# Kernel optimization log

Hardware: AMD Instinct MI355X
Metric: run time of the kernel (lower is better)

The kernel has to match this reference:

```python
import jax, jax.numpy as jnp
import numpy as np

B, DM, H, W = 2, 96, 48, 48
E = 192          # d_expand == d_inner
R, N = 6, 16     # delta_rank, d_state


def conv2d(x, w, b, groups=1, pad=0):
    out = jax.lax.conv_general_dilated(
        x, w, window_strides=(1, 1), padding=[(pad, pad), (pad, pad)],
        dimension_numbers=("NCHW", "OIHW", "NCHW"), feature_group_count=groups)
    return out + b[None, :, None, None]


def setup_inputs() -> dict:
    key = jax.random.key(0)
    ks = jax.random.split(key, 24)
    f = lambda k, shape, s: jax.random.normal(k, shape, jnp.float32) * s
    inp = {
        "x": jax.random.normal(ks[0], (B, DM, H, W), jnp.float32),
        "in_proj_w": f(ks[1], (2 * E, DM), 0.05),
        "conv_w": f(ks[2], (E, 1, 3, 3), 0.2),
        "conv_b": f(ks[3], (E,), 0.1),
        "x_proj_w": f(ks[4], (4, R + 2 * N, E), 0.01),
        "dt_proj_w": f(ks[5], (4, E, R), 0.01),
        "dt_proj_b": jnp.full((4, E), -9.0) + f(ks[6], (4, E), 0.1),
        "A_log": jnp.tile(jnp.log(jnp.arange(1, N + 1, dtype=jnp.float32))[None, None, :], (4, E, 1)),
        "Ds": jnp.ones((4, E), jnp.float32),
        "ln_g": jnp.ones(E, jnp.float32), "ln_b": jnp.zeros(E, jnp.float32),
        "c1_w": f(ks[7], (2 * E, E, 1, 1), 0.05), "c1_b": jnp.zeros(2 * E),
        "bn1_g": jnp.ones(2 * E), "bn1_b": jnp.zeros(2 * E), "bn1_m": jnp.zeros(2 * E), "bn1_v": jnp.ones(2 * E),
        "c2_w": f(ks[8], (2 * E, 1, 3, 3), 0.2), "c2_b": jnp.zeros(2 * E),
        "bn2_g": jnp.ones(2 * E), "bn2_b": jnp.zeros(2 * E), "bn2_m": jnp.zeros(2 * E), "bn2_v": jnp.ones(2 * E),
        "c3_w": f(ks[9], (E // 2, 2 * E, 1, 1), 0.05), "c3_b": jnp.zeros(E // 2),
        "se1_w": f(ks[10], (E // 4, E // 2), 0.1), "se1_b": jnp.zeros(E // 4),
        "se2_w": f(ks[11], (E // 2, E // 4), 0.1), "se2_b": jnp.zeros(E // 2),
    }
    return inp


def reference(x, in_proj_w, conv_w, conv_b, x_proj_w, dt_proj_w, dt_proj_b,
              A_log, Ds, ln_g, ln_b,
              c1_w, c1_b, bn1_g, bn1_b, bn1_m, bn1_v,
              c2_w, c2_b, bn2_g, bn2_b, bn2_m, bn2_v,
              c3_w, c3_b, se1_w, se1_b, se2_w, se2_b):
    Bs, _, Hs, Ws = x.shape
    L = Hs * Ws
    # in projection (Linear over channel dim), split x/z gates
    xz = jnp.einsum("bchw,oc->bohw", x, in_proj_w)
    xi, z = jnp.split(xz, 2, axis=1)
    # depthwise conv + SiLU
    xi = jax.nn.silu(conv2d(xi, conv_w, conv_b, groups=E, pad=1))
    # ---- selective scan (4-direction cross scan, cumsum formulation) ----
    xf = xi.reshape(Bs, E, L)
    xt = jnp.swapaxes(xi, 2, 3).reshape(Bs, E, L)
    xs = jnp.stack([xf, xf[..., ::-1], xt, xt[..., ::-1]], axis=1)  # [B,4,E,L]
    dbc = jnp.einsum("bkcl,krc->bkrl", xs, x_proj_w)                # [B,4,R+2N,L]
    dlt, b, c = dbc[:, :, :R], dbc[:, :, R:R + N], dbc[:, :, R + N:]
    dlt = jnp.einsum("bkrl,kdr->bkdl", dlt, dt_proj_w) + dt_proj_b[None, :, :, None]
    dlt = jax.nn.softplus(dlt)                                      # [B,4,E,L]
    dA = dlt[..., None] * A_log[None, :, :, None, :]                # [B,4,E,L,N]
    phi = jnp.exp(-jnp.cumsum(dA, axis=3))
    dbx = dlt[..., None] * jnp.swapaxes(b, 2, 3)[:, :, None] * xs[..., None]  # [B,4,E,L,N]
    h = phi * jnp.cumsum(dbx / (phi + 1e-12), axis=3)
    y = jnp.einsum("bkdln,bknl->bkdl", h, c) + Ds[None, :, :, None]  # [B,4,E,L]
    # ---- cross merge ----
    y1 = y[:, 0]
    y2 = y[:, 1, :, ::-1]
    y3 = jnp.swapaxes(y[:, 2].reshape(Bs, E, Ws, Hs), 2, 3).reshape(Bs, E, L)
    y4 = jnp.swapaxes(y[:, 3, :, ::-1].reshape(Bs, E, Ws, Hs), 2, 3).reshape(Bs, E, L)
    ys = (y1 + y2 + y3 + y4).reshape(Bs, E, Hs, Ws)
    # layernorm over channels
    yn = jnp.moveaxis(ys, 1, -1)
    mu = yn.mean(-1, keepdims=True)
    var = yn.var(-1, keepdims=True)
    yn = (yn - mu) / jnp.sqrt(var + 1e-5) * ln_g + ln_b
    u = jnp.moveaxis(yn, -1, 1) * z
    # ---- EFFN ----
    def bn(t, g, bb, m, v):
        return (t - m[None, :, None, None]) / jnp.sqrt(v + 1e-5)[None, :, None, None] * g[None, :, None, None] + bb[None, :, None, None]
    t = jax.nn.relu(bn(conv2d(u, c1_w, c1_b), bn1_g, bn1_b, bn1_m, bn1_v))
    t = jax.nn.relu(bn(conv2d(t, c2_w, c2_b, groups=2 * E, pad=1), bn2_g, bn2_b, bn2_m, bn2_v))
    t = conv2d(t, c3_w, c3_b)
    # squeeze-excitation: t + t * sigmoid(fc(relu(fc(avgpool(t)))))
    s = t.mean((2, 3))
    s = jax.nn.relu(s @ se1_w.T + se1_b)
    s = jax.nn.sigmoid(s @ se2_w.T + se2_b)
    return t + t * s[:, :, None, None]
```

## Files before the change

### kernel.cpp

```cpp
#include <hip/hip_runtime.h>
#include <hip/hip_bf16.h>

#define LTOT 2304
#define ECH  192
#define NCH  16
#define CCH  192
#define SCH  12

__device__ __forceinline__ int permS(int k, int l) {
  if (k == 0) return l;
  if (k == 1) return LTOT - 1 - l;
  int m = (k == 2) ? l : (LTOT - 1 - l);
  return (m % 48) * 48 + (m / 48);
}

__device__ __forceinline__ float sp_fast(float x) {
  float t = __expf(x);
  return (t <= 0.018f) ? t * fmaf(t, fmaf(t, 0.33333334f, -0.5f), 1.f) : log1pf(t);
}

__global__ __launch_bounds__(256) void k1_inproj(const float* __restrict__ x,
                                                 const float* __restrict__ W,
                                                 float* __restrict__ xi_pre,
                                                 float* __restrict__ z) {
  const int l0 = blockIdx.x * 32;
  const int o0 = blockIdx.y * 64;
  const int b  = blockIdx.z;
  __shared__ __align__(16) float xs[96 * 34];
  __shared__ __align__(16) float Wl[96 * 68];
  const int tid = threadIdx.x;
  for (int idx = tid; idx < 96 * 32; idx += 256) {
    int i = idx & 31, cc = idx >> 5;
    xs[cc * 34 + i] = x[(b * 96 + cc) * LTOT + l0 + i];
  }
  for (int idx = tid; idx < 64 * 96; idx += 256) {
    int r = idx / 96, cc = idx - r * 96;
    Wl[cc * 68 + r] = W[(o0 + r) * 96 + cc];
  }
  __syncthreads();
  const int lane = tid & 63, w = tid >> 6;
  const int jj = lane & 15, rqq = lane >> 4;
  const int rbase = 16 * w + 4 * rqq;
  float acc[2][4];
#pragma unroll
  for (int p = 0; p < 2; ++p)
#pragma unroll
    for (int t = 0; t < 4; ++t) acc[p][t] = 0.f;
#pragma unroll 4
  for (int cc = 0; cc < 96; ++cc) {
    const float4 wv = *(const float4*)&Wl[cc * 68 + rbase];
    const float2 xv = *(const float2*)&xs[cc * 34 + 2 * jj];
    acc[0][0] = fmaf(wv.x, xv.x, acc[0][0]); acc[0][1] = fmaf(wv.y, xv.x, acc[0][1]);
    acc[0][2] = fmaf(wv.z, xv.x, acc[0][2]); acc[0][3] = fmaf(wv.w, xv.x, acc[0][3]);
    acc[1][0] = fmaf(wv.x, xv.y, acc[1][0]); acc[1][1] = fmaf(wv.y, xv.y, acc[1][1]);
    acc[1][2] = fmaf(wv.z, xv.y, acc[1][2]); acc[1][3] = fmaf(wv.w, xv.y, acc[1][3]);
  }
  __syncthreads();
  float* ol = xs;
#pragma unroll
  for (int t = 0; t < 4; ++t) {
    ol[(rbase + t) * 33 + 2 * jj]     = acc[0][t];
    ol[(rbase + t) * 33 + 2 * jj + 1] = acc[1][t];
  }
  __syncthreads();
  for (int idx = tid; idx < 32 * 64; idx += 256) {
    int r = idx & 63, pos = idx >> 6;
    float v = ol[r * 33 + pos];
    int o = o0 + r, l = l0 + pos;
    if (o < ECH) xi_pre[(b * LTOT + l) * ECH + o] = v;
    else         z[(b * LTOT + l) * ECH + (o - ECH)] = v;
  }
}

__global__ __launch_bounds__(256) void k2_dwconv(const float* __restrict__ xi_pre,
                                                 const float* __restrict__ cw,
                                                 const float* __restrict__ cb,
                                                 float* __restrict__ xi) {
  int g = blockIdx.x * 256 + threadIdx.x;
  if (g >= 2 * LTOT * ECH) return;
  int e = g % ECH; int l = (g / ECH) % LTOT; int b = g / (ECH * LTOT);
  int h = l / 48, wq = l % 48;
  float acc = cb[e];
#pragma unroll
  for (int kh = 0; kh < 3; ++kh) {
    int hh = h + kh - 1; if (hh < 0 || hh >= 48) continue;
#pragma unroll
    for (int kw = 0; kw < 3; ++kw) {
      int ww = wq + kw - 1; if (ww < 0 || ww >= 48) continue;
      acc = fmaf(cw[e * 9 + kh * 3 + kw], xi_pre[(b * LTOT + hh * 48 + ww) * ECH + e], acc);
    }
  }
  xi[g] = acc / (1.f + __expf(-acc));
}

__global__ __launch_bounds__(256) void k3_xproj(const float* __restrict__ xi,
                                                const float* __restrict__ xw,
                                                float* __restrict__ dl6g,
                                                float* __restrict__ bT,
                                                float* __restrict__ cT) {
  const int l0 = blockIdx.x * 32;
  const int k  = blockIdx.y;
  const int b  = blockIdx.z;
  __shared__ __align__(16) float xs[96 * 34];
  __shared__ __align__(16) float Wl[192 * 40];
  const int tid = threadIdx.x;
  const float* wsrc = xw + k * 38 * ECH;
  for (int idx = tid; idx < 38 * 192; idx += 256) {
    int r = idx / 192, cc = idx - r * 192;
    Wl[cc * 40 + r] = wsrc[idx];
  }
  const int lane = tid & 63, w = tid >> 6;
  const int jj = lane & 15;
  const int rq = w * 4 + (lane >> 4);
  const int rqc = rq < 9 ? rq : 9;
  const int j0 = 2 * jj;
  float a00 = 0.f, a01 = 0.f, a02 = 0.f, a03 = 0.f;
  float a10 = 0.f, a11 = 0.f, a12 = 0.f, a13 = 0.f;
  for (int kc = 0; kc < 2; ++kc) {
    __syncthreads();
    for (int idx = tid; idx < 32 * 96; idx += 256) {
      int j = idx / 96, cc = idx - j * 96;
      int s = permS(k, l0 + j);
      xs[cc * 34 + j] = xi[(b * LTOT + s) * ECH + kc * 96 + cc];
    }
    __syncthreads();
#pragma unroll 4
    for (int cc = 0; cc < 96; ++cc) {
      const float2 xv = *(const float2*)&xs[cc * 34 + j0];
      const float4 wv = *(const float4*)&Wl[(kc * 96 + cc) * 40 + 4 * rqc];
      a00 = fmaf(wv.x, xv.x, a00); a01 = fmaf(wv.y, xv.x, a01);
      a02 = fmaf(wv.z, xv.x, a02); a03 = fmaf(wv.w, xv.x, a03);
      a10 = fmaf(wv.x, xv.y, a10); a11 = fmaf(wv.y, xv.y, a11);
      a12 = fmaf(wv.z, xv.y, a12); a13 = fmaf(wv.w, xv.y, a13);
    }
  }
  const int bk = b * 4 + k;
  if (rq < 10) {
    float av[2][4] = {{a00, a01, a02, a03}, {a10, a11, a12, a13}};
#pragma unroll
    for (int t = 0; t < 4; ++t) {
      int r = 4 * rq + t;
      if (r >= 38) continue;
#pragma unroll
      for (int p = 0; p < 2; ++p) {
        int j = j0 + p;
        float v = av[p][t];
        if (r < 6)       dl6g[((bk * LTOT) + l0 + j) * 6 + r] = v;
        else if (r < 22) bT[((bk * LTOT) + l0 + j) * NCH + (r - 6)] = v;
        else             cT[((bk * LTOT) + l0 + j) * NCH + (r - 22)] = v;
      }
    }
  }
}

__global__ __launch_bounds__(256) void k4a_scan1(const float* __restrict__ dl6g,
                                                 const float* __restrict__ xi,
                                                 const float* __restrict__ bT,
                                                 const float* __restrict__ Alog,
                                                 const float* __restrict__ dtw,
                                                 const float* __restrict__ dtb,
                                                 float* __restrict__ q,
                                                 float* __restrict__ Ts) {
  const int cb = blockIdx.x;
  const int db = blockIdx.y;
  const int bk = blockIdx.z;
  const int b = bk >> 2, k = bk & 3;
  const int l0 = cb * 48;
  __shared__ __align__(16) float2 sdx[48 * 64];
  __shared__ __align__(16) float  sb[48 * NCH];
  const int tid = threadIdx.x;
  const int dd = tid & 63, cg = tid >> 6;
  const int dg = db * 64 + dd;
  float b6 = dtb[k * ECH + dg];
  float w6[6];
  {
    const float2* d2 = (const float2*)(dtw + (k * ECH + dg) * 6);
    float2 u0 = d2[0], u1 = d2[1], u2 = d2[2];
    w6[0] = u0.x; w6[1] = u0.y; w6[2] = u1.x; w6[3] = u1.y; w6[4] = u2.x; w6[5] = u2.y;
  }
  for (int idx = tid; idx < 48 * NCH; idx += 256) sb[idx] = bT[(bk * LTOT + l0) * NCH + idx];
  for (int e = tid; e < 48 * 64; e += 256) {
    int s = e >> 6;
    const float* d6 = dl6g + (bk * LTOT + l0 + s) * 6;
    float xa = b6;
#pragma unroll
    for (int r = 0; r < 6; ++r) xa = fmaf(w6[r], d6[r], xa);
    float dl = sp_fast(xa);
    int sp = permS(k, l0 + s);
    sdx[s * 64 + dd] = make_float2(dl, xi[(b * LTOT + sp) * ECH + dg]);
  }
  float C1[16], h[16];
#pragma unroll
  for (int n = 0; n < 16; ++n) {
    C1[n] = Alog[(k * ECH + dg) * NCH + n];
    h[n] = 0.f;
  }
  __syncthreads();
  float Tsum = 0.f;
  for (int i = 0; i < SCH; ++i) {
    int j = cg * SCH + i;
    float2 dx = sdx[j * 64 + dd];
    float dl = dx.x;
    float u  = dl * dx.y;
    Tsum += dl;
    const float4* bb4 = (const float4*)(sb + j * NCH);
    float4 q0 = bb4[0], q1 = bb4[1], q2 = bb4[2], q3 = bb4[3];
    float bbl[16] = {q0.x, q0.y, q0.z, q0.w, q1.x, q1.y, q1.z, q1.w,
                     q2.x, q2.y, q2.z, q2.w, q3.x, q3.y, q3.z, q3.w};
    if (dl <= 0.018f) {
#pragma unroll
      for (int n = 0; n < 16; ++n) {
        float xn = C1[n] * dl;
        float e = fmaf(xn, fmaf(xn, fmaf(xn, -(1.f / 6.f), 0.5f), -1.f), 1.f);
        h[n] = fmaf(e, h[n], u * bbl[n]);
      }
    } else {
#pragma unroll
      for (int n = 0; n < 16; ++n) {
        float e = __expf(-C1[n] * dl);
        h[n] = fmaf(e, h[n], u * bbl[n]);
      }
    }
  }
  const int c = cb * 4 + cg;
  float4* qp = (float4*)(q + ((bk * CCH + c) * ECH + dg) * NCH);
  qp[0] = make_float4(h[0], h[1], h[2], h[3]);
  qp[1] = make_float4(h[4], h[5], h[6], h[7]);
  qp[2] = make_float4(h[8], h[9], h[10], h[11]);
  qp[3] = make_float4(h[12], h[13], h[14], h[15]);
  Ts[(bk * CCH + c) * ECH + dg] = Tsum;
}

__global__ __launch_bounds__(256) void k4b_comb(const float* __restrict__ Alog,
                                                const float* __restrict__ Ts,
                                                float* __restrict__ q) {
  int t = blockIdx.x * 256 + threadIdx.x;
  if (t >= 8 * ECH * NCH) return;
  int n = t & 15, d = (t >> 4) % ECH, bk = t / (NCH * ECH);
  int k = bk & 3;
  float A = Alog[(k * ECH + d) * NCH + n];
  float h = 0.f;
#pragma unroll 4
  for (int c = 0; c < CCH; ++c) {
    int base = ((bk * CCH + c) * ECH + d) * NCH + n;
    float qc = q[base];
    q[base] = h;
    float xv = A * Ts[(bk * CCH + c) * ECH + d];
    float P = (xv <= 0.05f)
                  ? fmaf(xv, fmaf(xv, fmaf(xv, -(1.f / 6.f), 0.5f), -1.f), 1.f)
                  : __expf(-xv);
    h = fmaf(P, h, qc);
  }
}

__global__ __launch_bounds__(256) void k4c_scan2(const float* __restrict__ dl6g,
                                                 const float* __restrict__ xi,
                                                 const float* __restrict__ bT,
                                                 const float* __restrict__ cT,
                                                 const float* __restrict__ Alog,
                                                 const float* __restrict__ dtw,
                                                 const float* __restrict__ dtb,
                                                 const float* __restrict__ hin,
                                                 float* __restrict__ yd) {
  const int cb = blockIdx.x;
  const int db = blockIdx.y;
  const int bk = blockIdx.z;
  const int b = bk >> 2, k = bk & 3;
  const int l0 = cb * 48;
  __shared__ __align__(16) float2 sdx[48 * 64];
  __shared__ __align__(16) float  sb[48 * NCH];
  __shared__ __align__(16) float  sc[48 * NCH];
  const int tid = threadIdx.x;
  const int dd = tid & 63, cg = tid >> 6;
  const int dg = db * 64 + dd;
  float b6 = dtb[k * ECH + dg];
  float w6[6];
  {
    const float2* d2 = (const float2*)(dtw + (k * ECH + dg) * 6);
    float2 u0 = d2[0], u1 = d2[1], u2 = d2[2];
    w6[0] = u0.x; w6[1] = u0.y; w6[2] = u1.x; w6[3] = u1.y; w6[4] = u2.x; w6[5] = u2.y;
  }
  for (int idx = tid; idx < 48 * NCH; idx += 256) {
    sb[idx] = bT[(bk * LTOT + l0) * NCH + idx];
    sc[idx] = cT[(bk * LTOT + l0) * NCH + idx];
  }
  for (int e = tid; e < 48 * 64; e += 256) {
    int s = e >> 6;
    const float* d6 = dl6g + (bk * LTOT + l0 + s) * 6;
    float xa = b6;
#pragma unroll
    for (int r = 0; r < 6; ++r) xa = fmaf(w6[r], d6[r], xa);
    float dl = sp_fast(xa);
    int sp = permS(k, l0 + s);
    sdx[s * 64 + dd] = make_float2(dl, xi[(b * LTOT + sp) * ECH + dg]);
  }
  float C1[16], h[16];
  const int c = cb * 4 + cg;
  const float4* hp = (const float4*)(hin + ((bk * CCH + c) * ECH + dg) * NCH);
  {
    float4 h0 = hp[0], h1 = hp[1], h2 = hp[2], h3 = hp[3];
    h[0]=h0.x; h[1]=h0.y; h[2]=h0.z; h[3]=h0.w;
    h[4]=h1.x; h[5]=h1.y; h[6]=h1.z; h[7]=h1.w;
    h[8]=h2.x; h[9]=h2.y; h[10]=h2.z; h[11]=h2.w;
    h[12]=h3.x; h[13]=h3.y; h[14]=h3.z; h[15]=h3.w;
  }
#pragma unroll
  for (int n = 0; n < 16; ++n) C1[n] = Alog[(k * ECH + dg) * NCH + n];
  float* ydk = yd + (b * 4 + k) * LTOT * ECH;
  __syncthreads();
  for (int i = 0; i < SCH; ++i) {
    int j = cg * SCH + i;
    float2 dx = sdx[j * 64 + dd];
    float dl = dx.x;
    float u  = dl * dx.y;
    const float4* bb4 = (const float4*)(sb + j * NCH);
    float4 q0 = bb4[0], q1 = bb4[1], q2 = bb4[2], q3 = bb4[3];
    float bbl[16] = {q0.x, q0.y, q0.z, q0.w, q1.x, q1.y, q1.z, q1.w,
                     q2.x, q2.y, q2.z, q2.w, q3.x, q3.y, q3.z, q3.w};
    if (dl <= 0.018f) {
#pragma unroll
      for (int n = 0; n < 16; ++n) {
        float xn = C1[n] * dl;
        float e = fmaf(xn, fmaf(xn, fmaf(xn, -(1.f / 6.f), 0.5f), -1.f), 1.f);
        h[n] = fmaf(e, h[n], u * bbl[n]);
      }
    } else {
#pragma unroll
      for (int n = 0; n < 16; ++n) {
        float e = __expf(-C1[n] * dl);
        h[n] = fmaf(e, h[n], u * bbl[n]);
      }
    }
    const float4* cc4 = (const float4*)(sc + j * NCH);
    float4 c0 = cc4[0], c1 = cc4[1], c2 = cc4[2], c3 = cc4[3];
    float ccl[16] = {c0.x, c0.y, c0.z, c0.w, c1.x, c1.y, c1.z, c1.w,
                     c2.x, c2.y, c2.z, c2.w, c3.x, c3.y, c3.z, c3.w};
    float y = 0.f;
#pragma unroll
    for (int n = 0; n < 16; ++n) y = fmaf(h[n], ccl[n], y);
    int sp = permS(k, l0 + j);
    ydk[sp * ECH + dg] = y;
  }
}

__global__ __launch_bounds__(256) void k5_ln(const float* __restrict__ yd,
                                             const float* __restrict__ Ds,
                                             const float* __restrict__ lng,
                                             const float* __restrict__ lnb,
                                             float* __restrict__ zu) {
  int p = blockIdx.x * 4 + (threadIdx.x >> 6);
  int lane = threadIdx.x & 63;
  int b = (p >= LTOT) ? 1 : 0;
  int l = p - b * LTOT;
  const float* y0 = yd + (b * 4) * LTOT * ECH + l * ECH;
  float vd[3], sd[3];
#pragma unroll
  for (int t = 0; t < 3; ++t) {
    int d = lane + t * 64;
    vd[t] = ((y0[d] + y0[LTOT * ECH + d]) + y0[2 * LTOT * ECH + d]) + y0[3 * LTOT * ECH + d];
    sd[t] = Ds[d] + Ds[ECH + d] + Ds[2 * ECH + d] + Ds[3 * ECH + d];
  }
  float s1 = vd[0] + vd[1] + vd[2];
  float s2 = sd[0] + sd[1] + sd[2];
#pragma unroll
  for (int off = 32; off > 0; off >>= 1) {
    s1 += __shfl_xor(s1, off, 64);
    s2 += __shfl_xor(s2, off, 64);
  }
  float mean_dot = s1 * (1.f / 192.f);
  float mean_sd  = s2 * (1.f / 192.f);
  float dev[3];
  float ss = 0.f;
#pragma unroll
  for (int t = 0; t < 3; ++t) {
    dev[t] = (vd[t] - mean_dot) + (sd[t] - mean_sd);
    ss = fmaf(dev[t], dev[t], ss);
  }
#pragma unroll
  for (int off = 32; off > 0; off >>= 1) ss += __shfl_xor(ss, off, 64);
  float rstd = 1.f / sqrtf(ss * (1.f / 192.f) + 1e-5f);
#pragma unroll
  for (int t = 0; t < 3; ++t) {
    int d = lane + t * 64;
    float yn = (dev[t] * rstd) * lng[d] + lnb[d];
    zu[p * ECH + d] = yn * zu[p * ECH + d];
  }
}

__global__ __launch_bounds__(256) void k6_c1(const float* __restrict__ u,
                                             const float* __restrict__ W,
                                             const float* __restrict__ c1b,
                                             const float* __restrict__ g1,
                                             const float* __restrict__ b1,
                                             const float* __restrict__ m1,
                                             const float* __restrict__ v1,
                                             float* __restrict__ t1,
                                             float* __restrict__ se) {
  const int l0 = blockIdx.x * 32;
  const int o0 = blockIdx.y * 64;
  const int b  = blockIdx.z;
  const int tid = threadIdx.x;
  if (blockIdx.x == 0 && blockIdx.y == 0 && blockIdx.z == 0 && tid < 192) se[tid] = 0.f;
  __shared__ __align__(16) float xs[96 * 34];
  __shared__ __align__(16) float Wl[96 * 68];
  const int lane = tid & 63, w = tid >> 6;
  const int jj = lane & 15, rqq = lane >> 4;
  const int rbase = 16 * w + 4 * rqq;
  float acc[2][4];
#pragma unroll
  for (int p = 0; p < 2; ++p)
#pragma unroll
    for (int t = 0; t < 4; ++t) acc[p][t] = 0.f;
  for (int kc = 0; kc < 2; ++kc) {
    if (kc) __syncthreads();
    for (int idx = tid; idx < 32 * 96; idx += 256) {
      int cc = idx % 96, i = idx / 96;
      xs[cc * 34 + i] = u[(b * LTOT + l0 + i) * ECH + kc * 96 + cc];
    }
    for (int idx = tid; idx < 64 * 96; idx += 256) {
      int r = idx / 96, cc = idx - r * 96;
      Wl[cc * 68 + r] = W[(o0 + r) * ECH + kc * 96 + cc];
    }
    __syncthreads();
#pragma unroll 4
    for (int cc = 0; cc < 96; ++cc) {
      const float4 wv = *(const float4*)&Wl[cc * 68 + rbase];
      const float2 xv = *(const float2*)&xs[cc * 34 + 2 * jj];
      acc[0][0] = fmaf(wv.x, xv.x, acc[0][0]); acc[0][1] = fmaf(wv.y, xv.x, acc[0][1]);
      acc[0][2] = fmaf(wv.z, xv.x, acc[0][2]); acc[0][3] = fmaf(wv.w, xv.x, acc[0][3]);
      acc[1][0] = fmaf(wv.x, xv.y, acc[1][0]); acc[1][1] = fmaf(wv.y, xv.y, acc[1][1]);
      acc[1][2] = fmaf(wv.z, xv.y, acc[1][2]); acc[1][3] = fmaf(wv.w, xv.y, acc[1][3]);
    }
  }
#pragma unroll
  for (int t = 0; t < 4; ++t) {
    int o = o0 + rbase + t;
    float sc = g1[o] / sqrtf(v1[o] + 1e-5f);
    float bias = (c1b[o] - m1[o]) * sc + b1[o];
#pragma unroll
    for (int p = 0; p < 2; ++p) acc[p][t] = fmaxf(fmaf(acc[p][t], sc, bias), 0.f);
  }
  __syncthreads();
  float* ol = xs;
#pragma unroll
  for (int t = 0; t < 4; ++t) {
    ol[(rbase + t) * 33 + 2 * jj]     = acc[0][t];
    ol[(rbase + t) * 33 + 2 * jj + 1] = acc[1][t];
  }
  __syncthreads();
  for (int idx = tid; idx < 32 * 64; idx += 256) {
    int pos = idx & 31, r = idx >> 5;
    t1[(b * 384 + o0 + r) * LTOT + l0 + pos] = ol[r * 33 + pos];
  }
}

__global__ __launch_bounds__(256) void k7_dw2(const float* __restrict__ t1,
                                              const float* __restrict__ cw,
                                              const float* __restrict__ cb,
                                              const float* __restrict__ g2,
                                              const float* __restrict__ b2,
                                              const float* __restrict__ m2,
                                              const float* __restrict__ v2,
                                              float* __restrict__ t2) {
  int g = blockIdx.x * 256 + threadIdx.x;
  if (g >= 2 * LTOT * 384) return;
  int l = g % LTOT; int o = (g / LTOT) % 384; int b = g / (LTOT * 384);
  int h = l / 48, wq = l % 48;
  const float* src = t1 + (b * 384 + o) * LTOT;
  float acc = cb[o];
#pragma unroll
  for (int kh = 0; kh < 3; ++kh) {
    int hh = h + kh - 1; if (hh < 0 || hh >= 48) continue;
#pragma unroll
    for (int kw = 0; kw < 3; ++kw) {
      int ww = wq + kw - 1; if (ww < 0 || ww >= 48) continue;
      acc = fmaf(cw[o * 9 + kh * 3 + kw], src[hh * 48 + ww], acc);
    }
  }
  float sc = g2[o] / sqrtf(v2[o] + 1e-5f);
  float val = (acc - m2[o]) * sc + b2[o];
  t2[g] = fmaxf(val, 0.f);
}

__global__ __launch_bounds__(256) void k8_c3(const float* __restrict__ t2,
                                             const float* __restrict__ W,
                                             const float* __restrict__ c3b,
                                             float* __restrict__ t3,
                                             float* __restrict__ se) {
  const int l0 = blockIdx.x * 32;
  const int r0 = blockIdx.y * 32;
  const int b  = blockIdx.z;
  __shared__ __align__(16) float Wl[384 * 34];
  __shared__ __align__(16) float xs[192 * 34];
  const int tid = threadIdx.x;
  const int lane = tid & 63, w = tid >> 6;
  const int jj = lane & 15, rqq = lane >> 4;
  const int rloc = 8 * w + 2 * rqq;
  for (int idx = tid; idx < 32 * 384; idx += 256) {
    int r = idx / 384, cc = idx - r * 384;
    Wl[cc * 34 + r] = W[(r0 + r) * 384 + cc];
  }
  float acc[2][2];
  acc[0][0] = acc[0][1] = acc[1][0] = acc[1][1] = 0.f;
  for (int kc = 0; kc < 2; ++kc) {
    if (kc) __syncthreads();
    for (int idx = tid; idx < 192 * 32; idx += 256) {
      int i = idx & 31, cc = idx >> 5;
      xs[cc * 34 + i] = t2[(b * 384 + kc * 192 + cc) * LTOT + l0 + i];
    }
    __syncthreads();
#pragma unroll 4
    for (int cc = 0; cc < 192; ++cc) {
      const float2 wv = *(const float2*)&Wl[(kc * 192 + cc) * 34 + rloc];
      const float2 xv = *(const float2*)&xs[cc * 34 + 2 * jj];
      acc[0][0] = fmaf(wv.x, xv.x, acc[0][0]); acc[0][1] = fmaf(wv.y, xv.x, acc[0][1]);
      acc[1][0] = fmaf(wv.x, xv.y, acc[1][0]); acc[1][1] = fmaf(wv.y, xv.y, acc[1][1]);
    }
  }
  {
    float b0 = c3b[r0 + rloc], b1v = c3b[r0 + rloc + 1];
    acc[0][0] += b0; acc[1][0] += b0; acc[0][1] += b1v; acc[1][1] += b1v;
  }
#pragma unroll
  for (int t = 0; t < 2; ++t) {
    float v = acc[0][t] + acc[1][t];
    v += __shfl_xor(v, 1); v += __shfl_xor(v, 2);
    v += __shfl_xor(v, 4); v += __shfl_xor(v, 8);
    if (jj == 0) atomicAdd(&se[b * 96 + r0 + rloc + t], v);
  }
  __syncthreads();
  float* ol = xs;
#pragma unroll
  for (int t = 0; t < 2; ++t) {
    ol[(rloc + t) * 33 + 2 * jj]     = acc[0][t];
    ol[(rloc + t) * 33 + 2 * jj + 1] = acc[1][t];
  }
  __syncthreads();
  for (int idx = tid; idx < 32 * 32; idx += 256) {
    int pos = idx & 31, r = idx >> 5;
    t3[(b * 96 + r0 + r) * LTOT + l0 + pos] = ol[r * 33 + pos];
  }
}

__global__ __launch_bounds__(256) void k9_out(const float* __restrict__ t3,
                                              const float* __restrict__ se,
                                              const float* __restrict__ w1,
                                              const float* __restrict__ sb1,
                                              const float* __restrict__ w2,
                                              const float* __restrict__ sb2,
                                              float* __restrict__ out) {
  __shared__ float sm[192];
  __shared__ float s1[96];
  __shared__ float smul[192];
  int t = threadIdx.x;
  if (t < 192) sm[t] = se[t] * (1.f / 2304.f);
  __syncthreads();
  if (t < 96) {
    int b = t / 48, i = t % 48;
    float a = sb1[i];
#pragma unroll 4
    for (int m = 0; m < 96; ++m) a = fmaf(w1[i * 96 + m], sm[b * 96 + m], a);
    s1[t] = fmaxf(a, 0.f);
  }
  __syncthreads();
  if (t < 192) {
    int b = t / 96, j = t % 96;
    float a = sb2[j];
#pragma unroll 4
    for (int i = 0; i < 48; ++i) a = fmaf(w2[j * 48 + i], s1[b * 48 + i], a);
    smul[t] = 1.f + 1.f / (1.f + __expf(-a));
  }
  __syncthreads();
  int g = blockIdx.x * 256 + t;
  if (g < 2 * 96 * LTOT) out[g] = t3[g] * smul[g / LTOT];
}

extern "C" void kernel_launch(void* const* d_in, const int* in_sizes, int n_in,
                              void* d_out, int out_size, void* d_ws, size_t ws_size,
                              hipStream_t stream) {
  const float* x     = (const float*)d_in[0];
  const float* inw   = (const float*)d_in[1];
  const float* convw = (const float*)d_in[2];
  const float* convb = (const float*)d_in[3];
  const float* xpw   = (const float*)d_in[4];
  const float* dtw   = (const float*)d_in[5];
  const float* dtb   = (const float*)d_in[6];
  const float* Alog  = (const float*)d_in[7];
  const float* Ds    = (const float*)d_in[8];
  const float* lng   = (const float*)d_in[9];
  const float* lnb   = (const float*)d_in[10];
  const float* c1w   = (const float*)d_in[11];
  const float* c1b   = (const float*)d_in[12];
  const float* bn1g  = (const float*)d_in[13];
  const float* bn1b  = (const float*)d_in[14];
  const float* bn1m  = (const float*)d_in[15];
  const float* bn1v  = (const float*)d_in[16];
  const float* c2w   = (const float*)d_in[17];
  const float* c2b   = (const float*)d_in[18];
  const float* bn2g  = (const float*)d_in[19];
  const float* bn2b  = (const float*)d_in[20];
  const float* bn2m  = (const float*)d_in[21];
  const float* bn2v  = (const float*)d_in[22];
  const float* c3w   = (const float*)d_in[23];
  const float* c3b   = (const float*)d_in[24];
  const float* se1w  = (const float*)d_in[25];
  const float* se1b  = (const float*)d_in[26];
  const float* se2w  = (const float*)d_in[27];
  const float* se2b  = (const float*)d_in[28];

  float* ws = (float*)d_ws;
  float* xi_pre = ws;
  float* z      = ws + 884736;
  float* xi     = ws + 1769472;
  float* dl6g   = ws + 2654208;
  float* bT     = ws + 2764800;
  float* cT     = ws + 3354624;
  float* q      = ws + 3944448;
  float* Ts     = ws + 13381632;
  float* se     = ws + 13676544;
  float* yd     = ws + 13676736;
  float* t1 = yd;
  float* t2 = yd + 1769472;
  float* t3 = q;

  k1_inproj<<<dim3(72, 6, 2), 256, 0, stream>>>(x, inw, xi_pre, z);
  k2_dwconv<<<3456, 256, 0, stream>>>(xi_pre, convw, convb, xi);
  k3_xproj<<<dim3(72, 4, 2), 256, 0, stream>>>(xi, xpw, dl6g, bT, cT);
  k4a_scan1<<<dim3(48, 3, 8), 256, 0, stream>>>(dl6g, xi, bT, Alog, dtw, dtb, q, Ts);
  k4b_comb<<<96, 256, 0, stream>>>(Alog, Ts, q);
  k4c_scan2<<<dim3(48, 3, 8), 256, 0, stream>>>(dl6g, xi, bT, cT, Alog, dtw, dtb, q, yd);
  k5_ln<<<1152, 256, 0, stream>>>(yd, Ds, lng, lnb, z);
  k6_c1<<<dim3(72, 6, 2), 256, 0, stream>>>(z, c1w, c1b, bn1g, bn1b, bn1m, bn1v, t1, se);
  k7_dw2<<<6912, 256, 0, stream>>>(t1, c2w, c2b, bn2g, bn2b, bn2m, bn2v, t2);
  k8_c3<<<dim3(72, 3, 2), 256, 0, stream>>>(t2, c3w, c3b, t3, se);
  k9_out<<<1728, 256, 0, stream>>>(t3, se, se1w, se1b, se2w, se2b, (float*)d_out);
}
```

Measured before the change: 341.6 us.

## Parallelize chunk-combine scan across chunk segments with two-level prefix in shared memory

The chunk-state combine kernel previously ran one thread per (bk,d,n) and walked all 192 chunks serially, using only 96 blocks. It now launches one block per (d,bk), splits the 192 chunks into 16 segments of 12 per thread, computes local decay products and partial states, combines segment prefixes through shared memory, then rewrites the carried-in states. This is meant to remove the long serial dependency chain and the low occupancy of that kernel. The cost is extra recomputation per thread, a serial loop over earlier segments, and strided global accesses that coalesce less well across d.

```diff
diff --git a/kernel.cpp b/kernel.cpp
--- a/kernel.cpp
+++ b/kernel.cpp
@@ -234,22 +234,42 @@
 __global__ __launch_bounds__(256) void k4b_comb(const float* __restrict__ Alog,
                                                 const float* __restrict__ Ts,
                                                 float* __restrict__ q) {
-  int t = blockIdx.x * 256 + threadIdx.x;
-  if (t >= 8 * ECH * NCH) return;
-  int n = t & 15, d = (t >> 4) % ECH, bk = t / (NCH * ECH);
-  int k = bk & 3;
-  float A = Alog[(k * ECH + d) * NCH + n];
-  float h = 0.f;
-#pragma unroll 4
-  for (int c = 0; c < CCH; ++c) {
-    int base = ((bk * CCH + c) * ECH + d) * NCH + n;
-    float qc = q[base];
-    q[base] = h;
-    float xv = A * Ts[(bk * CCH + c) * ECH + d];
-    float P = (xv <= 0.05f)
-                  ? fmaf(xv, fmaf(xv, fmaf(xv, -(1.f / 6.f), 0.5f), -1.f), 1.f)
-                  : __expf(-xv);
-    h = fmaf(P, h, qc);
+  const int d  = blockIdx.x;
+  const int bk = blockIdx.y;
+  const int k  = bk & 3;
+  const int tid = threadIdx.x;
+  const int n = tid & 15, seg = tid >> 4;
+  const float A = Alog[(k * ECH + d) * NCH + n];
+  const int c0 = seg * 12;
+  const float* tb = Ts + (bk * CCH + c0) * ECH + d;
+  float* qp = q + ((bk * CCH + c0) * ECH + d) * NCH + n;
+  float qv[12], P[12];
+#pragma unroll
+  for (int i = 0; i < 12; ++i) qv[i] = qp[i * (ECH * NCH)];
+#pragma unroll
+  for (int i = 0; i < 12; ++i) {
+    float xv = A * tb[i * ECH];
+    P[i] = (xv <= 0.05f)
+               ? fmaf(xv, fmaf(xv, fmaf(xv, -(1.f / 6.f), 0.5f), -1.f), 1.f)
+               : __expf(-xv);
+  }
+  float hl = 0.f, Pp = 1.f;
+#pragma unroll
+  for (int i = 0; i < 12; ++i) { hl = fmaf(P[i], hl, qv[i]); Pp *= P[i]; }
+  __shared__ float2 comb[16][17];
+  comb[seg][n] = make_float2(Pp, hl);
+  __syncthreads();
+  float H = 0.f;
+  for (int s = 0; s < seg; ++s) {
+    float2 cb = comb[s][n];
+    H = fmaf(cb.x, H, cb.y);
+  }
+  float h = H;
+#pragma unroll
+  for (int i = 0; i < 12; ++i) {
+    float hp = h;
+    h = fmaf(P[i], h, qv[i]);
+    qp[i * (ECH * NCH)] = hp;
   }
 }
 
@@ -627,7 +647,7 @@
   k2_dwconv<<<3456, 256, 0, stream>>>(xi_pre, convw, convb, xi);
   k3_xproj<<<dim3(72, 4, 2), 256, 0, stream>>>(xi, xpw, dl6g, bT, cT);
   k4a_scan1<<<dim3(48, 3, 8), 256, 0, stream>>>(dl6g, xi, bT, Alog, dtw, dtb, q, Ts);
-  k4b_comb<<<96, 256, 0, stream>>>(Alog, Ts, q);
+  k4b_comb<<<dim3(192, 8), 256, 0, stream>>>(Alog, Ts, q);
   k4c_scan2<<<dim3(48, 3, 8), 256, 0, stream>>>(dl6g, xi, bT, cT, Alog, dtw, dtb, q, yd);
   k5_ln<<<1152, 256, 0, stream>>>(yd, Ds, lng, lnb, z);
   k6_c1<<<dim3(72, 6, 2), 256, 0, stream>>>(z, c1w, c1b, bn1g, bn1b, bn1m, bn1v, t1, se);
```

After: 301.0 us. -11.9%, faster.
